# Kernel tuning notes

Hardware: AMD Instinct MI355X
Metric: run time of the kernel (lower is better)

## Reference

```python
import jax, jax.numpy as jnp
import numpy as np

E = 1024
H = 16
D = E // H
S = 2048
B = 2

def setup_inputs() -> dict:
    key = jax.random.key(0)
    ks = jax.random.split(key, 5)
    x = jax.random.normal(ks[0], (B, S, E), dtype=jnp.float32)
    W_qkv = jax.random.normal(ks[1], (E, 3 * E), dtype=jnp.float32) / np.sqrt(E)
    b_qkv = jax.random.normal(ks[2], (3 * E,), dtype=jnp.float32) * 0.02
    W_out = jax.random.normal(ks[3], (E, E), dtype=jnp.float32) / np.sqrt(E)
    b_out = jax.random.normal(ks[4], (E,), dtype=jnp.float32) * 0.02
    return {"x": x, "W_qkv": W_qkv, "b_qkv": b_qkv, "W_out": W_out, "b_out": b_out}

def reference(x, W_qkv, b_qkv, W_out, b_out):
    b, s, e = x.shape
    qkv = x @ W_qkv + b_qkv                      # [B,S,3E]
    q, k, v = jnp.split(qkv, 3, axis=-1)
    # [B,S,E] -> [B,H,S,D]
    q = q.reshape(b, s, H, D).transpose(0, 2, 1, 3)
    k = k.reshape(b, s, H, D).transpose(0, 2, 1, 3)
    v = v.reshape(b, s, H, D).transpose(0, 2, 1, 3)
    scale = 1.0 / np.sqrt(D)
    att = jnp.einsum('bhqd,bhkd->bhqk', q, k) * scale
    causal = jnp.tril(jnp.ones((s, s), dtype=bool))
    att = jnp.where(causal[None, None], att, -jnp.inf)
    att = jax.nn.softmax(att, axis=-1)
    out = jnp.einsum('bhqk,bhkd->bhqd', att, v)  # [B,H,S,D]
    out = out.transpose(0, 2, 1, 3).reshape(b, s, e)
    return out @ W_out + b_out
```

## Files before the change

kernel.cpp:

```cpp
#include <hip/hip_runtime.h>

typedef unsigned short u16;
typedef __bf16  bf16x8 __attribute__((ext_vector_type(8)));
typedef float   f32x4  __attribute__((ext_vector_type(4)));
typedef unsigned int   u32x4 __attribute__((ext_vector_type(4)));
typedef unsigned short u16x4 __attribute__((ext_vector_type(4)));
typedef unsigned short u16x8 __attribute__((ext_vector_type(8)));

#define BB 2
#define HH 16
#define DD 64
#define SS 2048
#define EE 1024

#define BM 128
#define BN 128

#define QSCALE 0.1803368801111244f

static __device__ __forceinline__ u16 f2bf(float f) {
    unsigned int u = __float_as_uint(f);
    u += 0x7FFFu + ((u >> 16) & 1u);
    return (u16)(u >> 16);
}

union BfCast { u32x4 u; bf16x8 b; };
static __device__ __forceinline__ bf16x8 ldb8(const u16* p) {
    BfCast x; x.u = *(const u32x4*)p; return x.b;
}

static __device__ __forceinline__ void gload16(const u16* g, u16* l) {
    __builtin_amdgcn_global_load_lds(
        (const __attribute__((address_space(1))) unsigned int*)g,
        (__attribute__((address_space(3))) unsigned int*)l, 16, 0, 0);
}

static __device__ __forceinline__ int fidx(int m, int k) {
    return (((m >> 4) * 32 + (k >> 5)) * 512) + ((((k >> 3) & 3) * 16 + (m & 15)) * 8) + (k & 7);
}
static __device__ __forceinline__ int kidx(int s, int d) {
    return (((s >> 4) * 2 + (d >> 5)) * 512) + ((((d >> 3) & 3) * 16 + (s & 15)) * 8) + (d & 7);
}
static __device__ __forceinline__ int vidx(int key, int d) {
    return (((key >> 5) * 4 + (d >> 4)) * 512) + ((((key >> 3) & 3) * 16 + (d & 15)) * 8) + (key & 7);
}

__global__ __launch_bounds__(256) void conv_frag_kernel(
    const float* __restrict__ in, u16* __restrict__ out)
{
    const int t = blockIdx.x * 256 + threadIdx.x;
    const int u = t >> 6;
    const int w = t & 63;
    const int m = (u >> 5) * 16 + (w & 15);
    const int k = (u & 31) * 32 + (w >> 4) * 8;
    const float* p = in + m * 1024 + k;
    const f32x4 a = *(const f32x4*)p;
    const f32x4 b = *(const f32x4*)(p + 4);
    u16x8 o;
    o[0] = f2bf(a[0]); o[1] = f2bf(a[1]); o[2] = f2bf(a[2]); o[3] = f2bf(a[3]);
    o[4] = f2bf(b[0]); o[5] = f2bf(b[1]); o[6] = f2bf(b[2]); o[7] = f2bf(b[3]);
    *(u16x8*)&out[u * 512 + w * 8] = o;
}

__global__ __launch_bounds__(256) void transpose_frag_kernel(
    const float* __restrict__ in, u16* __restrict__ out, int C)
{
    __shared__ float tile[32][33];
    const int tx = threadIdx.x & 31;
    const int ty = threadIdx.x >> 5;
    const int ct = C >> 5;
    const int bc = blockIdx.x % ct;
    const int br = blockIdx.x / ct;
    const int c0 = bc * 32, r0 = br * 32;
    #pragma unroll
    for (int i = 0; i < 4; i++)
        tile[ty + i * 8][tx] = in[(r0 + ty + i * 8) * C + c0 + tx];
    __syncthreads();
    #pragma unroll
    for (int i = 0; i < 4; i++) {
        const int n = c0 + ty + i * 8;
        out[((n >> 4) * 32 + (r0 >> 5)) * 512 + (((tx >> 3) & 3) * 16 + (n & 15)) * 8 + (tx & 7)]
            = f2bf(tile[tx][ty + i * 8]);
    }
}

__global__ __launch_bounds__(256) void gemm_qkv_kernel(
    const u16* __restrict__ Af,
    const u16* __restrict__ Bf,
    const float* __restrict__ bias,
    u16* __restrict__ Qb, u16* __restrict__ Kb, u16* __restrict__ Vb)
{
    __shared__ __align__(16) u16 As[2][BM * 32];
    __shared__ __align__(16) u16 Bs[2][BN * 32];
    const int lane = threadIdx.x & 63;
    const int wave = threadIdx.x >> 6;
    const int nb = 3 * EE / BN;
    const int tm = blockIdx.x / nb, tn = blockIdx.x % nb;
    const int lm = lane & 15, quad = lane >> 4;
    const int UG = 32 * 512;

    const u16* ag = Af + (tm * 8 + 2 * wave) * UG + lane * 8;
    const u16* bg = Bf + (tn * 8 + 2 * wave) * UG + lane * 8;
    const int ld = wave * 1024;

    const int wy = wave >> 1, wx = wave & 1;
    f32x4 acc[4][4] = {};

    gload16(ag,      &As[0][ld]);
    gload16(ag + UG, &As[0][ld + 512]);
    gload16(bg,      &Bs[0][ld]);
    gload16(bg + UG, &Bs[0][ld + 512]);
    ag += 512; bg += 512;

    for (int it = 0; it < 32; ++it) {
        const int cur = it & 1;
        __syncthreads();
        if (it + 1 < 32) {
            gload16(ag,      &As[cur ^ 1][ld]);
            gload16(ag + UG, &As[cur ^ 1][ld + 512]);
            gload16(bg,      &Bs[cur ^ 1][ld]);
            gload16(bg + UG, &Bs[cur ^ 1][ld + 512]);
            ag += 512; bg += 512;
        }
        bf16x8 af[4], bf[4];
        #pragma unroll
        for (int i = 0; i < 4; i++) {
            af[i] = ldb8(&As[cur][(wy * 4 + i) * 512 + lane * 8]);
            bf[i] = ldb8(&Bs[cur][(wx * 4 + i) * 512 + lane * 8]);
        }
        #pragma unroll
        for (int mi = 0; mi < 4; mi++)
            #pragma unroll
            for (int ni = 0; ni < 4; ni++)
                acc[mi][ni] = __builtin_amdgcn_mfma_f32_16x16x32_bf16(af[mi], bf[ni], acc[mi][ni], 0, 0, 0);
    }

    const int gm0 = tm * BM + wy * 64;
    const int gn0 = tn * BN + wx * 64;
    #pragma unroll
    for (int ni = 0; ni < 4; ni++) {
        const int n = gn0 + ni * 16 + lm;
        const float bv = bias[n];
        const int which = n >> 10;
        const int e = n & 1023;
        const int h = e >> 6, d = e & 63;
        #pragma unroll
        for (int mi = 0; mi < 4; mi++) {
            if (which == 2) {
                const int m0 = gm0 + mi * 16 + quad * 4;
                const int b = m0 >> 11, key0 = m0 & 2047;
                u16x4 pk;
                #pragma unroll
                for (int r = 0; r < 4; r++) pk[r] = f2bf(acc[mi][ni][r] + bv);
                *(u16x4*)&Vb[(b * HH + h) * 131072 + vidx(key0, d)] = pk;
            } else if (which == 1) {
                #pragma unroll
                for (int r = 0; r < 4; r++) {
                    const int m = gm0 + mi * 16 + quad * 4 + r;
                    const int b = m >> 11, s = m & 2047;
                    Kb[(b * HH + h) * 131072 + kidx(s, d)] = f2bf(acc[mi][ni][r] + bv);
                }
            } else {
                #pragma unroll
                for (int r = 0; r < 4; r++) {
                    const int m = gm0 + mi * 16 + quad * 4 + r;
                    const int b = m >> 11, s = m & 2047;
                    Qb[((b * HH + h) * SS + s) * DD + d] = f2bf((acc[mi][ni][r] + bv) * QSCALE);
                }
            }
        }
    }
}

__global__ __launch_bounds__(256) void attn_kernel(
    const u16* __restrict__ Qb, const u16* __restrict__ Kb,
    const u16* __restrict__ Vb, u16* __restrict__ Ob)
{
    __shared__ __align__(16) u16 Ks[2][4096];
    __shared__ __align__(16) u16 Vs[2][4096];
    __shared__ __align__(16) u16 Plds[4 * 16 * 72];
    const int tid = threadIdx.x;
    const int lane = tid & 63, wave = tid >> 6;
    const int lm = lane & 15, quad = lane >> 4;
    const int bh = blockIdx.x & 31;
    const int qt = (SS / 64 - 1) - (blockIdx.x >> 5);
    const int q0 = qt * 64;
    const int qrow = q0 + wave * 16;
    const int b = bh >> 4, h = bh & 15;

    const u16* qbase = Qb + (bh * SS + qrow) * DD;
    const bf16x8 qf0 = ldb8(qbase + lm * DD + quad * 8);
    const bf16x8 qf1 = ldb8(qbase + lm * DD + 32 + quad * 8);

    const u16* ktile = Kb + bh * 131072;
    const u16* vtile = Vb + bh * 131072;
    u16* Pw = Plds + wave * (16 * 72);

    BfCast oc; oc.u = (u32x4){0x3F803F80u, 0x3F803F80u, 0x3F803F80u, 0x3F803F80u};
    const bf16x8 ones = oc.b;

    f32x4 oacc[4] = {};
    f32x4 lacc = {0.f, 0.f, 0.f, 0.f};

    const int ktmax = qt + 1;
    {
        const u16* kg = ktile + wave * 1024 + lane * 8;
        const u16* vg = vtile + wave * 1024 + lane * 8;
        gload16(kg,       &Ks[0][wave * 1024]);
        gload16(kg + 512, &Ks[0][wave * 1024 + 512]);
        gload16(vg,       &Vs[0][wave * 1024]);
        gload16(vg + 512, &Vs[0][wave * 1024 + 512]);
    }
    for (int kt = 0; kt < ktmax; ++kt) {
        const int cur = kt & 1;
        const int k0 = kt * 64;
        __syncthreads();
        if (kt + 1 < ktmax) {
            const u16* kg = ktile + (kt + 1) * 4096 + wave * 1024 + lane * 8;
            const u16* vg = vtile + (kt + 1) * 4096 + wave * 1024 + lane * 8;
            gload16(kg,       &Ks[cur ^ 1][wave * 1024]);
            gload16(kg + 512, &Ks[cur ^ 1][wave * 1024 + 512]);
            gload16(vg,       &Vs[cur ^ 1][wave * 1024]);
            gload16(vg + 512, &Vs[cur ^ 1][wave * 1024 + 512]);
        }

        f32x4 s[4];
        #pragma unroll
        for (int g = 0; g < 4; g++) {
            f32x4 z = {0.f, 0.f, 0.f, 0.f};
            z    = __builtin_amdgcn_mfma_f32_16x16x32_bf16(ldb8(&Ks[cur][(g * 2) * 512 + lane * 8]), qf0, z, 0, 0, 0);
            s[g] = __builtin_amdgcn_mfma_f32_16x16x32_bf16(ldb8(&Ks[cur][(g * 2 + 1) * 512 + lane * 8]), qf1, z, 0, 0, 0);
        }
        if (k0 + 63 > qrow) {
            const int lim = qrow + lm - k0 - quad * 4;
            #pragma unroll
            for (int g = 0; g < 4; g++)
                #pragma unroll
                for (int r = 0; r < 4; r++)
                    if (g * 16 + r > lim) s[g][r] = -INFINITY;
        }
        #pragma unroll
        for (int g = 0; g < 4; g++) {
            u16x4 pk;
            #pragma unroll
            for (int r = 0; r < 4; r++) pk[r] = f2bf(__builtin_amdgcn_exp2f(s[g][r]));
            *(u16x4*)&Pw[lm * 72 + g * 16 + quad * 4] = pk;
        }
        const bf16x8 pf0 = ldb8(&Pw[lm * 72 + quad * 8]);
        const bf16x8 pf1 = ldb8(&Pw[lm * 72 + 32 + quad * 8]);
        lacc = __builtin_amdgcn_mfma_f32_16x16x32_bf16(ones, pf0, lacc, 0, 0, 0);
        lacc = __builtin_amdgcn_mfma_f32_16x16x32_bf16(ones, pf1, lacc, 0, 0, 0);
        #pragma unroll
        for (int dg = 0; dg < 4; dg++) {
            oacc[dg] = __builtin_amdgcn_mfma_f32_16x16x32_bf16(ldb8(&Vs[cur][dg * 512 + lane * 8]), pf0, oacc[dg], 0, 0, 0);
            oacc[dg] = __builtin_amdgcn_mfma_f32_16x16x32_bf16(ldb8(&Vs[cur][(4 + dg) * 512 + lane * 8]), pf1, oacc[dg], 0, 0, 0);
        }
    }
    const float inv = 1.0f / lacc[0];
    u16* ob = Ob + (((b * SS + qrow) >> 4) * 32 + h * 2) * 512;
    #pragma unroll
    for (int dg = 0; dg < 4; dg++) {
        u16x4 pk;
        #pragma unroll
        for (int r = 0; r < 4; r++) pk[r] = f2bf(oacc[dg][r] * inv);
        *(u16x4*)&ob[(dg >> 1) * 512 + (((dg * 2 + (quad >> 1)) & 3) * 16 + lm) * 8 + (quad & 1) * 4] = pk;
    }
}

__global__ __launch_bounds__(256) void gemm_out_kernel(
    const u16* __restrict__ Af,
    const u16* __restrict__ Bf,
    const float* __restrict__ bias,
    float* __restrict__ Out)
{
    __shared__ __align__(16) u16 As[2][BM * 32];
    __shared__ __align__(16) u16 Bs[2][BN * 32];
    const int lane = threadIdx.x & 63;
    const int wave = threadIdx.x >> 6;
    const int nb = EE / BN;
    const int tm = blockIdx.x / nb, tn = blockIdx.x % nb;
    const int lm = lane & 15, quad = lane >> 4;
    const int UG = 32 * 512;

    const u16* ag = Af + (tm * 8 + 2 * wave) * UG + lane * 8;
    const u16* bg = Bf + (tn * 8 + 2 * wave) * UG + lane * 8;
    const int ld = wave * 1024;

    const int wy = wave >> 1, wx = wave & 1;
    f32x4 acc[4][4] = {};

    gload16(ag,      &As[0][ld]);
    gload16(ag + UG, &As[0][ld + 512]);
    gload16(bg,      &Bs[0][ld]);
    gload16(bg + UG, &Bs[0][ld + 512]);
    ag += 512; bg += 512;

    for (int it = 0; it < 32; ++it) {
        const int cur = it & 1;
        __syncthreads();
        if (it + 1 < 32) {
            gload16(ag,      &As[cur ^ 1][ld]);
            gload16(ag + UG, &As[cur ^ 1][ld + 512]);
            gload16(bg,      &Bs[cur ^ 1][ld]);
            gload16(bg + UG, &Bs[cur ^ 1][ld + 512]);
            ag += 512; bg += 512;
        }
        bf16x8 af[4], bf[4];
        #pragma unroll
        for (int i = 0; i < 4; i++) {
            af[i] = ldb8(&As[cur][(wy * 4 + i) * 512 + lane * 8]);
            bf[i] = ldb8(&Bs[cur][(wx * 4 + i) * 512 + lane * 8]);
        }
        #pragma unroll
        for (int mi = 0; mi < 4; mi++)
            #pragma unroll
            for (int ni = 0; ni < 4; ni++)
                acc[mi][ni] = __builtin_amdgcn_mfma_f32_16x16x32_bf16(af[mi], bf[ni], acc[mi][ni], 0, 0, 0);
    }

    const int gm0 = tm * BM + wy * 64;
    const int gn0 = tn * BN + wx * 64;
    #pragma unroll
    for (int ni = 0; ni < 4; ni++) {
        const int n = gn0 + ni * 16 + lm;
        const float bv = bias[n];
        #pragma unroll
        for (int mi = 0; mi < 4; mi++)
            #pragma unroll
            for (int r = 0; r < 4; r++)
                Out[(gm0 + mi * 16 + quad * 4 + r) * EE + n] = acc[mi][ni][r] + bv;
    }
}

extern "C" void kernel_launch(void* const* d_in, const int* in_sizes, int n_in,
                              void* d_out, int out_size, void* d_ws, size_t ws_size,
                              hipStream_t stream)
{
    const float* x     = (const float*)d_in[0];
    const float* Wqkv  = (const float*)d_in[1];
    const float* bqkv  = (const float*)d_in[2];
    const float* Wout  = (const float*)d_in[3];
    const float* bout  = (const float*)d_in[4];
    float* out = (float*)d_out;

    char* ws = (char*)d_ws;
    u16* xb    = (u16*)(ws + 0);
    u16* wqkvT = (u16*)(ws + 8388608);
    u16* woutT = (u16*)(ws + 14680064);
    u16* Qb    = (u16*)(ws + 16777216);
    u16* Kb    = (u16*)(ws + 25165824);
    u16* Vb    = (u16*)(ws + 33554432);
    u16* Ob    = (u16*)(ws + 41943040);
    if (ws_size < 50331648) return;

    conv_frag_kernel<<<2048, 256, 0, stream>>>(x, xb);
    transpose_frag_kernel<<<(EE / 32) * (3 * EE / 32), 256, 0, stream>>>(Wqkv, wqkvT, 3 * EE);
    transpose_frag_kernel<<<(EE / 32) * (EE / 32), 256, 0, stream>>>(Wout, woutT, EE);
    gemm_qkv_kernel<<<(BB * SS / BM) * (3 * EE / BN), 256, 0, stream>>>(xb, wqkvT, bqkv, Qb, Kb, Vb);
    attn_kernel<<<BB * HH * (SS / 64), 256, 0, stream>>>(Qb, Kb, Vb, Ob);
    gemm_out_kernel<<<(BB * SS / BM) * (EE / BN), 256, 0, stream>>>(Ob, woutT, bout, out);
}
```

Baseline: 185.1 us.

## Merge prep kernels into one launch and shrink GEMM tiles for more blocks

Combines the x conversion and both weight transposes into a single prep kernel dispatched by block index, removing two launches. Shrinks the QKV GEMM tile to 64x128 and the output GEMM tile to 64x64, with a unified shared buffer where each wave loads a share of the A and B fragments. The aim is more blocks in flight to fill the CUs, at the cost of less operand reuse per tile and more global traffic.

Measured after the change: 173.9 us. 1.06x faster.

```diff
diff --git a/kernel.cpp b/kernel.cpp
--- a/kernel.cpp
+++ b/kernel.cpp
@@ -13,9 +13,6 @@
 #define SS 2048
 #define EE 1024
 
-#define BM 128
-#define BN 128
-
 #define QSCALE 0.1803368801111244f
 
 static __device__ __forceinline__ u16 f2bf(float f) {
@@ -35,9 +32,7 @@
         (__attribute__((address_space(3))) unsigned int*)l, 16, 0, 0);
 }
 
-static __device__ __forceinline__ int fidx(int m, int k) {
-    return (((m >> 4) * 32 + (k >> 5)) * 512) + ((((k >> 3) & 3) * 16 + (m & 15)) * 8) + (k & 7);
-}
+#define UG (32 * 512)
 static __device__ __forceinline__ int kidx(int s, int d) {
     return (((s >> 4) * 2 + (d >> 5)) * 512) + ((((d >> 3) & 3) * 16 + (s & 15)) * 8) + (d & 7);
 }
@@ -45,32 +40,34 @@
     return (((key >> 5) * 4 + (d >> 4)) * 512) + ((((key >> 3) & 3) * 16 + (d & 15)) * 8) + (key & 7);
 }
 
-__global__ __launch_bounds__(256) void conv_frag_kernel(
-    const float* __restrict__ in, u16* __restrict__ out)
-{
-    const int t = blockIdx.x * 256 + threadIdx.x;
-    const int u = t >> 6;
-    const int w = t & 63;
-    const int m = (u >> 5) * 16 + (w & 15);
-    const int k = (u & 31) * 32 + (w >> 4) * 8;
-    const float* p = in + m * 1024 + k;
-    const f32x4 a = *(const f32x4*)p;
-    const f32x4 b = *(const f32x4*)(p + 4);
-    u16x8 o;
-    o[0] = f2bf(a[0]); o[1] = f2bf(a[1]); o[2] = f2bf(a[2]); o[3] = f2bf(a[3]);
-    o[4] = f2bf(b[0]); o[5] = f2bf(b[1]); o[6] = f2bf(b[2]); o[7] = f2bf(b[3]);
-    *(u16x8*)&out[u * 512 + w * 8] = o;
-}
-
-__global__ __launch_bounds__(256) void transpose_frag_kernel(
-    const float* __restrict__ in, u16* __restrict__ out, int C)
+__global__ __launch_bounds__(256) void prep_kernel(
+    const float* __restrict__ x,    u16* __restrict__ xb,
+    const float* __restrict__ Wqkv, u16* __restrict__ wqkvT,
+    const float* __restrict__ Wout, u16* __restrict__ woutT)
 {
     __shared__ float tile[32][33];
+    const int bid = blockIdx.x;
+    if (bid < 2048) {
+        const int t = bid * 256 + threadIdx.x;
+        const int u = t >> 6, w = t & 63;
+        const int m = (u >> 5) * 16 + (w & 15);
+        const int k = (u & 31) * 32 + (w >> 4) * 8;
+        const float* p = x + m * 1024 + k;
+        const f32x4 a = *(const f32x4*)p;
+        const f32x4 b = *(const f32x4*)(p + 4);
+        u16x8 o;
+        o[0] = f2bf(a[0]); o[1] = f2bf(a[1]); o[2] = f2bf(a[2]); o[3] = f2bf(a[3]);
+        o[4] = f2bf(b[0]); o[5] = f2bf(b[1]); o[6] = f2bf(b[2]); o[7] = f2bf(b[3]);
+        *(u16x8*)&xb[u * 512 + w * 8] = o;
+        return;
+    }
+    const float* in; u16* out; int C, tb;
+    if (bid < 2048 + 3072) { in = Wqkv; out = wqkvT; C = 3072; tb = bid - 2048; }
+    else                   { in = Wout; out = woutT; C = 1024; tb = bid - 5120; }
     const int tx = threadIdx.x & 31;
     const int ty = threadIdx.x >> 5;
     const int ct = C >> 5;
-    const int bc = blockIdx.x % ct;
-    const int br = blockIdx.x / ct;
+    const int bc = tb % ct, br = tb / ct;
     const int c0 = bc * 32, r0 = br * 32;
     #pragma unroll
     for (int i = 0; i < 4; i++)
@@ -90,53 +87,56 @@
     const float* __restrict__ bias,
     u16* __restrict__ Qb, u16* __restrict__ Kb, u16* __restrict__ Vb)
 {
-    __shared__ __align__(16) u16 As[2][BM * 32];
-    __shared__ __align__(16) u16 Bs[2][BN * 32];
+    __shared__ __align__(16) u16 Us[2][12 * 512];
     const int lane = threadIdx.x & 63;
     const int wave = threadIdx.x >> 6;
-    const int nb = 3 * EE / BN;
+    const int nb = 3 * EE / 128;
     const int tm = blockIdx.x / nb, tn = blockIdx.x % nb;
     const int lm = lane & 15, quad = lane >> 4;
-    const int UG = 32 * 512;
-
-    const u16* ag = Af + (tm * 8 + 2 * wave) * UG + lane * 8;
-    const u16* bg = Bf + (tn * 8 + 2 * wave) * UG + lane * 8;
-    const int ld = wave * 1024;
+
+    const u16* sp[3];
+    #pragma unroll
+    for (int j = 0; j < 3; j++) {
+        const int idx = 3 * wave + j;
+        sp[j] = (idx < 4) ? (Af + (tm * 4 + idx) * UG + lane * 8)
+                          : (Bf + (tn * 8 + idx - 4) * UG + lane * 8);
+    }
+    u16* ld0 = &Us[0][3 * wave * 512];
+    u16* ld1 = &Us[1][3 * wave * 512];
 
     const int wy = wave >> 1, wx = wave & 1;
-    f32x4 acc[4][4] = {};
-
-    gload16(ag,      &As[0][ld]);
-    gload16(ag + UG, &As[0][ld + 512]);
-    gload16(bg,      &Bs[0][ld]);
-    gload16(bg + UG, &Bs[0][ld + 512]);
-    ag += 512; bg += 512;
+    f32x4 acc[2][4] = {};
+
+    gload16(sp[0], ld0);
+    gload16(sp[1], ld0 + 512);
+    gload16(sp[2], ld0 + 1024);
 
     for (int it = 0; it < 32; ++it) {
         const int cur = it & 1;
         __syncthreads();
         if (it + 1 < 32) {
-            gload16(ag,      &As[cur ^ 1][ld]);
-            gload16(ag + UG, &As[cur ^ 1][ld + 512]);
-            gload16(bg,      &Bs[cur ^ 1][ld]);
-            gload16(bg + UG, &Bs[cur ^ 1][ld + 512]);
-            ag += 512; bg += 512;
-        }
-        bf16x8 af[4], bf[4];
-        #pragma unroll
-        for (int i = 0; i < 4; i++) {
-            af[i] = ldb8(&As[cur][(wy * 4 + i) * 512 + lane * 8]);
-            bf[i] = ldb8(&Bs[cur][(wx * 4 + i) * 512 + lane * 8]);
-        }
-        #pragma unroll
-        for (int mi = 0; mi < 4; mi++)
+            u16* ld = cur ? ld0 : ld1;
+            const int ko = (it + 1) * 512;
+            gload16(sp[0] + ko, ld);
+            gload16(sp[1] + ko, ld + 512);
+            gload16(sp[2] + ko, ld + 1024);
+        }
+        bf16x8 af[2], bf[4];
+        #pragma unroll
+        for (int i = 0; i < 2; i++)
+            af[i] = ldb8(&Us[cur][(wy * 2 + i) * 512 + lane * 8]);
+        #pragma unroll
+        for (int i = 0; i < 4; i++)
+            bf[i] = ldb8(&Us[cur][(4 + wx * 4 + i) * 512 + lane * 8]);
+        #pragma unroll
+        for (int mi = 0; mi < 2; mi++)
             #pragma unroll
             for (int ni = 0; ni < 4; ni++)
                 acc[mi][ni] = __builtin_amdgcn_mfma_f32_16x16x32_bf16(af[mi], bf[ni], acc[mi][ni], 0, 0, 0);
     }
 
-    const int gm0 = tm * BM + wy * 64;
-    const int gn0 = tn * BN + wx * 64;
+    const int gm0 = tm * 64 + wy * 32;
+    const int gn0 = tn * 128 + wx * 64;
     #pragma unroll
     for (int ni = 0; ni < 4; ni++) {
         const int n = gn0 + ni * 16 + lm;
@@ -145,7 +145,7 @@
         const int e = n & 1023;
         const int h = e >> 6, d = e & 63;
         #pragma unroll
-        for (int mi = 0; mi < 4; mi++) {
+        for (int mi = 0; mi < 2; mi++) {
             if (which == 2) {
                 const int m0 = gm0 + mi * 16 + quad * 4;
                 const int b = m0 >> 11, key0 = m0 & 2047;
@@ -273,59 +273,59 @@
     const float* __restrict__ bias,
     float* __restrict__ Out)
 {
-    __shared__ __align__(16) u16 As[2][BM * 32];
-    __shared__ __align__(16) u16 Bs[2][BN * 32];
+    __shared__ __align__(16) u16 Us[2][8 * 512];
     const int lane = threadIdx.x & 63;
     const int wave = threadIdx.x >> 6;
-    const int nb = EE / BN;
+    const int nb = EE / 64;
     const int tm = blockIdx.x / nb, tn = blockIdx.x % nb;
     const int lm = lane & 15, quad = lane >> 4;
-    const int UG = 32 * 512;
-
-    const u16* ag = Af + (tm * 8 + 2 * wave) * UG + lane * 8;
-    const u16* bg = Bf + (tn * 8 + 2 * wave) * UG + lane * 8;
-    const int ld = wave * 1024;
+
+    const u16* sp[2];
+    #pragma unroll
+    for (int j = 0; j < 2; j++) {
+        const int idx = 2 * wave + j;
+        sp[j] = (idx < 4) ? (Af + (tm * 4 + idx) * UG + lane * 8)
+                          : (Bf + (tn * 4 + idx - 4) * UG + lane * 8);
+    }
+    u16* ld0 = &Us[0][2 * wave * 512];
+    u16* ld1 = &Us[1][2 * wave * 512];
 
     const int wy = wave >> 1, wx = wave & 1;
-    f32x4 acc[4][4] = {};
-
-    gload16(ag,      &As[0][ld]);
-    gload16(ag + UG, &As[0][ld + 512]);
-    gload16(bg,      &Bs[0][ld]);
-    gload16(bg + UG, &Bs[0][ld + 512]);
-    ag += 512; bg += 512;
+    f32x4 acc[2][2] = {};
+
+    gload16(sp[0], ld0);
+    gload16(sp[1], ld0 + 512);
 
     for (int it = 0; it < 32; ++it) {
         const int cur = it & 1;
         __syncthreads();
         if (it + 1 < 32) {
-            gload16(ag,      &As[cur ^ 1][ld]);
-            gload16(ag + UG, &As[cur ^ 1][ld + 512]);
-            gload16(bg,      &Bs[cur ^ 1][ld]);
-            gload16(bg + UG, &Bs[cur ^ 1][ld + 512]);
-            ag += 512; bg += 512;
-        }
-        bf16x8 af[4], bf[4];
-        #pragma unroll
-        for (int i = 0; i < 4; i++) {
-            af[i] = ldb8(&As[cur][(wy * 4 + i) * 512 + lane * 8]);
-            bf[i] = ldb8(&Bs[cur][(wx * 4 + i) * 512 + lane * 8]);
-        }
-        #pragma unroll
-        for (int mi = 0; mi < 4; mi++)
-            #pragma unroll
-            for (int ni = 0; ni < 4; ni++)
+            u16* ld = cur ? ld0 : ld1;
+            const int ko = (it + 1) * 512;
+            gload16(sp[0] + ko, ld);
+            gload16(sp[1] + ko, ld + 512);
+        }
+        bf16x8 af[2], bf[2];
+        #pragma unroll
+        for (int i = 0; i < 2; i++) {
+            af[i] = ldb8(&Us[cur][(wy * 2 + i) * 512 + lane * 8]);
+            bf[i] = ldb8(&Us[cur][(4 + wx * 2 + i) * 512 + lane * 8]);
+        }
+        #pragma unroll
+        for (int mi = 0; mi < 2; mi++)
+            #pragma unroll
+            for (int ni = 0; ni < 2; ni++)
                 acc[mi][ni] = __builtin_amdgcn_mfma_f32_16x16x32_bf16(af[mi], bf[ni], acc[mi][ni], 0, 0, 0);
     }
 
-    const int gm0 = tm * BM + wy * 64;
-    const int gn0 = tn * BN + wx * 64;
-    #pragma unroll
-    for (int ni = 0; ni < 4; ni++) {
+    const int gm0 = tm * 64 + wy * 32;
+    const int gn0 = tn * 64 + wx * 32;
+    #pragma unroll
+    for (int ni = 0; ni < 2; ni++) {
         const int n = gn0 + ni * 16 + lm;
         const float bv = bias[n];
         #pragma unroll
-        for (int mi = 0; mi < 4; mi++)
+        for (int mi = 0; mi < 2; mi++)
             #pragma unroll
             for (int r = 0; r < 4; r++)
                 Out[(gm0 + mi * 16 + quad * 4 + r) * EE + n] = acc[mi][ni][r] + bv;
@@ -353,10 +353,8 @@
     u16* Ob    = (u16*)(ws + 41943040);
     if (ws_size < 50331648) return;
 
-    conv_frag_kernel<<<2048, 256, 0, stream>>>(x, xb);
-    transpose_frag_kernel<<<(EE / 32) * (3 * EE / 32), 256, 0, stream>>>(Wqkv, wqkvT, 3 * EE);
-    transpose_frag_kernel<<<(EE / 32) * (EE / 32), 256, 0, stream>>>(Wout, woutT, EE);
-    gemm_qkv_kernel<<<(BB * SS / BM) * (3 * EE / BN), 256, 0, stream>>>(xb, wqkvT, bqkv, Qb, Kb, Vb);
+    prep_kernel<<<2048 + 3072 + 1024, 256, 0, stream>>>(x, xb, Wqkv, wqkvT, Wout, woutT);
+    gemm_qkv_kernel<<<(BB * SS / 64) * (3 * EE / 128), 256, 0, stream>>>(xb, wqkvT, bqkv, Qb, Kb, Vb);
     attn_kernel<<<BB * HH * (SS / 64), 256, 0, stream>>>(Qb, Kb, Vb, Ob);
-    gemm_out_kernel<<<(BB * SS / BM) * (EE / BN), 256, 0, stream>>>(Ob, woutT, bout, out);
-}
+    gemm_out_kernel<<<(BB * SS / 64) * (EE / 64), 256, 0, stream>>>(Ob, woutT, bout, out);
+}
```
